# Kernel optimization log

Measured on AMD Instinct MI355X. Metric: run time of the kernel, lower is better.

## Reference

```python
import jax, jax.numpy as jnp
import numpy as np

N, C = 16384, 512

def setup_inputs() -> dict:
    key = jax.random.key(0)
    k1, k2 = jax.random.split(key)
    mean = jax.random.normal(k1, (N, C), dtype=jnp.float32)
    var = jax.random.uniform(k2, (N, C), dtype=jnp.float32)  # positive diagonal variances
    return {"mean": mean, "var": var, "num_samples": 400}

def reference(mean, var, num_samples):
    # Monte Carlo estimate of E[softmax(mean + eps)], eps ~ N(0, diag(var)).
    # lax.scan keeps memory flat (no [S, N, C] buffer), matching the torch loop.
    std = jnp.sqrt(var)
    keys = jax.random.split(jax.random.key(42), num_samples)

    def body(acc, k):
        eps = jax.random.normal(k, mean.shape, dtype=mean.dtype) * std
        return acc + jax.nn.softmax(mean + eps, axis=-1), None

    acc, _ = jax.lax.scan(body, jnp.zeros_like(mean), keys)
    return acc / num_samples
```

## Files before the change

### kernel.cpp

```cpp
#include <hip/hip_runtime.h>
#include <stdint.h>

#define NSAMP 400
#define NC 512

#if __has_builtin(__builtin_amdgcn_exp2f)
#define EXP2F(x) __builtin_amdgcn_exp2f(x)
#else
#define EXP2F(x) __expf((x) * 0.6931471805599453f)
#endif
#if __has_builtin(__builtin_amdgcn_logf)
#define LOG2F(x) __builtin_amdgcn_logf(x)
#else
#define LOG2F(x) (__logf(x) * 1.4426950408889634f)
#endif

static __device__ __forceinline__ uint32_t rotl32(uint32_t v, int n) {
  return (v << n) | (v >> (32 - n));
}

#define TFS(x0, x1, R) { x0 += x1; x1 = rotl32(x1, R); x1 ^= x0; }
static __device__ __forceinline__ void threefry2x32_full(
    uint32_t k0, uint32_t k1, uint32_t x0, uint32_t x1,
    uint32_t& o0, uint32_t& o1)
{
  const uint32_t ks2 = k0 ^ k1 ^ 0x1BD11BDAu;
  x0 += k0; x1 += k1;
  TFS(x0,x1,13) TFS(x0,x1,15) TFS(x0,x1,26) TFS(x0,x1, 6)
  x0 += k1; x1 += ks2 + 1u;
  TFS(x0,x1,17) TFS(x0,x1,29) TFS(x0,x1,16) TFS(x0,x1,24)
  x0 += ks2; x1 += k0 + 2u;
  TFS(x0,x1,13) TFS(x0,x1,15) TFS(x0,x1,26) TFS(x0,x1, 6)
  x0 += k0; x1 += k1 + 3u;
  TFS(x0,x1,17) TFS(x0,x1,29) TFS(x0,x1,16) TFS(x0,x1,24)
  x0 += k1; x1 += ks2 + 4u;
  TFS(x0,x1,13) TFS(x0,x1,15) TFS(x0,x1,26) TFS(x0,x1, 6)
  x0 += ks2; x1 += k0 + 5u;
  o0 = x0; o1 = x1;
}

#define R3OP(R)          { x0 += x1; x1 = rotl32(x1, R) ^ x0; }
#define INJR(ka, kb, R)  { x1 += kb; x0 = x0 + x1 + ka; x1 = rotl32(x1, R) ^ x0; }

static __device__ __forceinline__ uint32_t tf_bits_fused(
    uint32_t k0, uint32_t k1, uint32_t ks2,
    uint32_t I1, uint32_t I2, uint32_t I3, uint32_t I4, uint32_t I5,
    uint32_t cnt)
{
  uint32_t x1 = cnt + k1;
  uint32_t x0 = x1 + k0;
  x1 = rotl32(x1, 13) ^ x0;
  R3OP(15) R3OP(26) R3OP(6)
  INJR(k1,  I1, 17) R3OP(29) R3OP(16) R3OP(24)
  INJR(ks2, I2, 13) R3OP(15) R3OP(26) R3OP(6)
  INJR(k0,  I3, 17) R3OP(29) R3OP(16) R3OP(24)
  INJR(k1,  I4, 13) R3OP(15) R3OP(26) R3OP(6)
  x0 += ks2; x1 += I5;
  return x0 ^ x1;
}

static __device__ __forceinline__ float softexp(float u, float L, float sd2, float m2) {
  float p;
  if (L > -7.2134752f) {
    float w = fmaf(L, -0.69314718f, -2.5f);
    p =              2.81022636e-08f;
    p = fmaf(p, w,   3.43273939e-07f);
    p = fmaf(p, w,  -3.5233877e-06f);
    p = fmaf(p, w,  -4.39150654e-06f);
    p = fmaf(p, w,   0.00021858087f);
    p = fmaf(p, w,  -0.00125372503f);
    p = fmaf(p, w,  -0.00417768164f);
    p = fmaf(p, w,   0.246640727f);
    p = fmaf(p, w,   1.50140941f);
  } else {
    float w = __builtin_amdgcn_sqrtf(L * -0.69314718f) - 3.0f;
    p =             -0.000200214257f;
    p = fmaf(p, w,   0.000100950558f);
    p = fmaf(p, w,   0.00134934322f);
    p = fmaf(p, w,  -0.00367342844f);
    p = fmaf(p, w,   0.00573950773f);
    p = fmaf(p, w,  -0.0076224613f);
    p = fmaf(p, w,   0.00943887047f);
    p = fmaf(p, w,   1.00167406f);
    p = fmaf(p, w,   2.83297682f);
  }
  float px = p * u;
  return EXP2F(fmaf(px, sd2, m2));
}

__global__ __launch_bounds__(256)
void mc_softmax_kernel(const float* __restrict__ mean,
                       const float* __restrict__ var,
                       float* __restrict__ out)
{
  __shared__ __align__(16) uint32_t kc[NSAMP][8];
  for (int s = threadIdx.x; s < NSAMP; s += 256) {
    uint32_t a, b;
    threefry2x32_full(0u, 42u, 0u, (uint32_t)s, a, b);
    uint32_t ks2 = a ^ b ^ 0x1BD11BDAu;
    kc[s][0] = a;        kc[s][1] = b;
    kc[s][2] = ks2;      kc[s][3] = ks2 + 1u;
    kc[s][4] = a + 2u;   kc[s][5] = b + 3u;
    kc[s][6] = ks2 + 4u; kc[s][7] = a + 5u;
  }
  __syncthreads();

  const int lane  = threadIdx.x & 63;
  const int row   = (blockIdx.x << 2) + (threadIdx.x >> 6);
  const int cbase = lane << 2;

  const float* mr = mean + (size_t)row * NC;
  const float* vr = var  + (size_t)row * NC;

  float m2[8], sd2[8], acc[8];
  {
    const float L2E = 1.4426950408889634f;
    const float S2L = 2.0402788959f;
    float4 t0 = *(const float4*)(mr + cbase);
    float4 t1 = *(const float4*)(mr + 256 + cbase);
    m2[0] = t0.x * L2E; m2[1] = t0.y * L2E; m2[2] = t0.z * L2E; m2[3] = t0.w * L2E;
    m2[4] = t1.x * L2E; m2[5] = t1.y * L2E; m2[6] = t1.z * L2E; m2[7] = t1.w * L2E;
    float4 v0 = *(const float4*)(vr + cbase);
    float4 v1 = *(const float4*)(vr + 256 + cbase);
    sd2[0] = __builtin_amdgcn_sqrtf(v0.x) * S2L;
    sd2[1] = __builtin_amdgcn_sqrtf(v0.y) * S2L;
    sd2[2] = __builtin_amdgcn_sqrtf(v0.z) * S2L;
    sd2[3] = __builtin_amdgcn_sqrtf(v0.w) * S2L;
    sd2[4] = __builtin_amdgcn_sqrtf(v1.x) * S2L;
    sd2[5] = __builtin_amdgcn_sqrtf(v1.y) * S2L;
    sd2[6] = __builtin_amdgcn_sqrtf(v1.z) * S2L;
    sd2[7] = __builtin_amdgcn_sqrtf(v1.w) * S2L;
  }
#pragma unroll
  for (int j = 0; j < 8; ++j) acc[j] = 0.0f;

  const uint32_t base = (uint32_t)(row * NC + cbase);
  const float lo = -0.99999994f;

  for (int s = 0; s < NSAMP; ++s) {
    const uint4 ca = *(const uint4*)&kc[s][0];
    const uint4 cb = *(const uint4*)&kc[s][4];
    const uint32_t k0 = ca.x, k1 = ca.y, ks2 = ca.z, I1 = ca.w;
    const uint32_t I2 = cb.x, I3 = cb.y, I4 = cb.z, I5 = cb.w;

    float u8[8], L8[8];
#pragma unroll
    for (int j = 0; j < 8; ++j) {
      const uint32_t cnt = base + (uint32_t)(j < 4 ? j : 252 + j);
      uint32_t bits = tf_bits_fused(k0, k1, ks2, I1, I2, I3, I4, I5, cnt);
      float f = __uint_as_float(__builtin_amdgcn_alignbit(0x7Fu, bits, 9u)) - 1.0f;
      float u = fmaf(f, 2.0f, lo);
      u8[j] = u;
      L8[j] = LOG2F(fmaf(u, -u, 1.0f));
    }

    float e8[8], sum = 0.0f;
#pragma unroll
    for (int j = 0; j < 8; ++j) {
      e8[j] = softexp(u8[j], L8[j], sd2[j], m2[j]);
      sum += e8[j];
    }

#pragma unroll
    for (int off = 32; off >= 1; off >>= 1)
      sum += __shfl_xor(sum, off);
    const float inv = __builtin_amdgcn_rcpf(sum);
#pragma unroll
    for (int j = 0; j < 8; ++j)
      acc[j] = fmaf(e8[j], inv, acc[j]);
  }

  float* orow = out + (size_t)row * NC;
  const float sc = 1.0f / (float)NSAMP;
  float4 o0, o1;
  o0.x = acc[0] * sc; o0.y = acc[1] * sc; o0.z = acc[2] * sc; o0.w = acc[3] * sc;
  o1.x = acc[4] * sc; o1.y = acc[5] * sc; o1.z = acc[6] * sc; o1.w = acc[7] * sc;
  *(float4*)(orow + cbase)       = o0;
  *(float4*)(orow + 256 + cbase) = o1;
}

extern "C" void kernel_launch(void* const* d_in, const int* in_sizes, int n_in,
                              void* d_out, int out_size, void* d_ws, size_t ws_size,
                              hipStream_t stream) {
  const float* mean = (const float*)d_in[0];
  const float* var  = (const float*)d_in[1];
  float* out        = (float*)d_out;

  const int rows = out_size / NC;
  const int blocks = rows / 4;
  mc_softmax_kernel<<<blocks, 256, 0, stream>>>(mean, var, out);
}
```

Before: 6.780 ms.

## Use DPP wave reduction, scalarize sample keys, and interleave two samples per iteration

Replaces the shfl_xor butterfly reduction with a DPP row-shift/broadcast chain ending in a readlane, so the softmax normalizer is computed without LDS-backed shuffles. The per-sample Threefry keys are moved to scalar registers with readfirstlane, and the loop handles two samples per iteration, interleaving one sample's reduction with the other's RNG and exp work to hide latency. This raises register pressure, and the pairing assumes an even sample count.

```diff
diff --git a/kernel.cpp b/kernel.cpp
--- a/kernel.cpp
+++ b/kernel.cpp
@@ -57,6 +57,12 @@
   INJR(k1,  I4, 13) R3OP(15) R3OP(26) R3OP(6)
   x0 += ks2; x1 += I5;
   return x0 ^ x1;
+}
+
+static __device__ __forceinline__ void bits2uL(uint32_t bits, float& u, float& L) {
+  float f = __uint_as_float(__builtin_amdgcn_alignbit(0x7Fu, bits, 9u)) - 1.0f;
+  u = fmaf(f, 2.0f, -0.99999994f);
+  L = LOG2F(fmaf(u, -u, 1.0f));
 }
 
 static __device__ __forceinline__ float softexp(float u, float L, float sd2, float m2) {
@@ -88,6 +94,25 @@
   return EXP2F(fmaf(px, sd2, m2));
 }
 
+static __device__ __forceinline__ uint32_t rfl(uint32_t x) {
+  return (uint32_t)__builtin_amdgcn_readfirstlane((int)x);
+}
+
+template <int CTRL>
+static __device__ __forceinline__ float dppadd(float x) {
+  return x + __int_as_float(
+      __builtin_amdgcn_update_dpp(0, __float_as_int(x), CTRL, 0xf, 0xf, false));
+}
+static __device__ __forceinline__ float wave_sum_bcast(float x) {
+  x = dppadd<0x111>(x);
+  x = dppadd<0x112>(x);
+  x = dppadd<0x114>(x);
+  x = dppadd<0x118>(x);
+  x = dppadd<0x142>(x);
+  x = dppadd<0x143>(x);
+  return __uint_as_float((uint32_t)__builtin_amdgcn_readlane(__float_as_int(x), 63));
+}
+
 __global__ __launch_bounds__(256)
 void mc_softmax_kernel(const float* __restrict__ mean,
                        const float* __restrict__ var,
@@ -135,39 +160,48 @@
   for (int j = 0; j < 8; ++j) acc[j] = 0.0f;
 
   const uint32_t base = (uint32_t)(row * NC + cbase);
-  const float lo = -0.99999994f;
-
-  for (int s = 0; s < NSAMP; ++s) {
-    const uint4 ca = *(const uint4*)&kc[s][0];
-    const uint4 cb = *(const uint4*)&kc[s][4];
-    const uint32_t k0 = ca.x, k1 = ca.y, ks2 = ca.z, I1 = ca.w;
-    const uint32_t I2 = cb.x, I3 = cb.y, I4 = cb.z, I5 = cb.w;
-
-    float u8[8], L8[8];
+  uint32_t cnt[8];
+#pragma unroll
+  for (int j = 0; j < 4; ++j) { cnt[j] = base + (uint32_t)j; cnt[4+j] = base + 256u + (uint32_t)j; }
+
+  for (int s = 0; s < NSAMP; s += 2) {
+    const uint4 a0 = *(const uint4*)&kc[s][0];
+    const uint4 a1 = *(const uint4*)&kc[s][4];
+    const uint4 b0 = *(const uint4*)&kc[s + 1][0];
+    const uint4 b1 = *(const uint4*)&kc[s + 1][4];
+    const uint32_t Ak0 = rfl(a0.x), Ak1 = rfl(a0.y), Aks = rfl(a0.z), AI1 = rfl(a0.w);
+    const uint32_t AI2 = rfl(a1.x), AI3 = rfl(a1.y), AI4 = rfl(a1.z), AI5 = rfl(a1.w);
+    const uint32_t Bk0 = rfl(b0.x), Bk1 = rfl(b0.y), Bks = rfl(b0.z), BI1 = rfl(b0.w);
+    const uint32_t BI2 = rfl(b1.x), BI3 = rfl(b1.y), BI4 = rfl(b1.z), BI5 = rfl(b1.w);
+
+    float uA[8], LA[8];
 #pragma unroll
     for (int j = 0; j < 8; ++j) {
-      const uint32_t cnt = base + (uint32_t)(j < 4 ? j : 252 + j);
-      uint32_t bits = tf_bits_fused(k0, k1, ks2, I1, I2, I3, I4, I5, cnt);
-      float f = __uint_as_float(__builtin_amdgcn_alignbit(0x7Fu, bits, 9u)) - 1.0f;
-      float u = fmaf(f, 2.0f, lo);
-      u8[j] = u;
-      L8[j] = LOG2F(fmaf(u, -u, 1.0f));
+      uint32_t bits = tf_bits_fused(Ak0, Ak1, Aks, AI1, AI2, AI3, AI4, AI5, cnt[j]);
+      bits2uL(bits, uA[j], LA[j]);
     }
-
-    float e8[8], sum = 0.0f;
+    float eA[8], sA = 0.0f;
+#pragma unroll
+    for (int j = 0; j < 8; ++j) { eA[j] = softexp(uA[j], LA[j], sd2[j], m2[j]); sA += eA[j]; }
+
+    float uB[8], LB[8];
 #pragma unroll
     for (int j = 0; j < 8; ++j) {
-      e8[j] = softexp(u8[j], L8[j], sd2[j], m2[j]);
-      sum += e8[j];
+      uint32_t bits = tf_bits_fused(Bk0, Bk1, Bks, BI1, BI2, BI3, BI4, BI5, cnt[j]);
+      bits2uL(bits, uB[j], LB[j]);
     }
 
-#pragma unroll
-    for (int off = 32; off >= 1; off >>= 1)
-      sum += __shfl_xor(sum, off);
-    const float inv = __builtin_amdgcn_rcpf(sum);
-#pragma unroll
-    for (int j = 0; j < 8; ++j)
-      acc[j] = fmaf(e8[j], inv, acc[j]);
+    const float invA = __builtin_amdgcn_rcpf(wave_sum_bcast(sA));
+#pragma unroll
+    for (int j = 0; j < 8; ++j) acc[j] = fmaf(eA[j], invA, acc[j]);
+
+    float eB[8], sB = 0.0f;
+#pragma unroll
+    for (int j = 0; j < 8; ++j) { eB[j] = softexp(uB[j], LB[j], sd2[j], m2[j]); sB += eB[j]; }
+
+    const float invB = __builtin_amdgcn_rcpf(wave_sum_bcast(sB));
+#pragma unroll
+    for (int j = 0; j < 8; ++j) acc[j] = fmaf(eB[j], invB, acc[j]);
   }
 
   float* orow = out + (size_t)row * NC;
```

Result: faster. 6.575 ms (-3.0%).
